# Performance work log

Hardware: AMD Instinct MI355X
Metric: run time of the kernel (lower is better)

Reference implementation:

```python
import jax, jax.numpy as jnp
import numpy as np

B, T, D_IN, N, O = 64, 512, 256, 1024, 128


def setup_inputs() -> dict:
    key = jax.random.key(0)
    k1, k2, k3, k4, k5 = jax.random.split(key, 5)
    X = jax.random.normal(k1, (B, T, D_IN), dtype=jnp.float32)
    # scale recurrent/input weights so tanh does not fully saturate
    Win = jax.random.normal(k2, (D_IN, N), dtype=jnp.float32) / np.sqrt(D_IN)
    W = jax.random.normal(k3, (N, N), dtype=jnp.float32) / np.sqrt(N)
    Wout = jax.random.normal(k4, (N, O), dtype=jnp.float32) / np.sqrt(N)
    bout = jax.random.normal(k5, (O,), dtype=jnp.float32)
    return {"X": X, "Win": Win, "W": W, "Wout": Wout, "bout": bout}


def reference(X, Win, W, Wout, bout):
    # Faithful to Model.evaluate:
    #   s[:, 0] = 0
    #   out = s @ Wout + bout
    b, t, _ = X.shape
    n = W.shape[0]
    s0 = jnp.zeros((b, n), dtype=X.dtype)

    def step(s, x):  # s: [B,N], x: [B,D_in]
        s_new = jnp.tanh(s @ W + x @ Win)
        return s_new, s_new

    xs = jnp.swapaxes(X[:, : t - 1, :], 0, 1)  # [T-1, B, D_in]
    _, s_seq = jax.lax.scan(step, s0, xs)  # [T-1, B, N]
    s = jnp.concatenate([s0[None], s_seq], axis=0)  # [T, B, N]
    s = jnp.swapaxes(s, 0, 1)  # [B, T, N]
    out = s @ Wout + bout  # [B, T, O]
    return (s, out)
```

## Files before the change

kernel.cpp:

```cpp
#include <hip/hip_runtime.h>

#define B_ 64
#define T_ 512
#define DIN_ 256
#define N_ 1024
#define O_ 128

using half8 = __attribute__((ext_vector_type(8))) _Float16;
using f32x4 = __attribute__((ext_vector_type(4))) float;
typedef unsigned long long ull;

__device__ __forceinline__ half8 cvt8(float4 a, float4 b) {
    half8 h;
    h[0] = (_Float16)a.x; h[1] = (_Float16)a.y; h[2] = (_Float16)a.z; h[3] = (_Float16)a.w;
    h[4] = (_Float16)b.x; h[5] = (_Float16)b.y; h[6] = (_Float16)b.z; h[7] = (_Float16)b.w;
    return h;
}

__device__ __forceinline__ float fast_tanh(float x) {
    float ax = __builtin_fabsf(x);
    float e  = __expf(-2.0f * ax);
    float r  = __fdividef(1.0f - e, 1.0f + e);
    return x < 0.0f ? -r : r;
}

__global__ void init_kernel(unsigned int* sent) {
    sent[threadIdx.x] = 0u;
}

__global__ __launch_bounds__(512, 1) void rnn_kernel(
    const float* __restrict__ X,
    const float* __restrict__ W,
    const float* __restrict__ Win,
    float* __restrict__ s_out,
    _Float16* __restrict__ exch,
    unsigned int* __restrict__ sent)
{
    const int bs   = blockIdx.x & 3;
    const int cg   = blockIdx.x >> 2;
    const int tid  = threadIdx.x;
    const int wave = tid >> 6;
    const int lane = tid & 63;
    const int l15  = lane & 15;
    const int quad = lane >> 4;
    const int col0 = cg * 128 + wave * 16;
    const int arow = bs * 16 + l15;
    const int crow = bs * 16 + quad * 4;

    __shared__ _Float16 slab[16 * 1032];

    half8 wf[32];
    for (int p = 0; p < 8; ++p) {
        const int c = tid & 15, k0 = tid >> 4;
        const int wc = cg * 128 + p * 16 + c;
        for (int k = k0; k < N_; k += 32)
            slab[c * 1032 + k] = (_Float16)W[(size_t)k * N_ + wc];
        __syncthreads();
        if (wave == p) {
            #pragma unroll
            for (int kb = 0; kb < 32; ++kb)
                wf[kb] = *(const half8*)&slab[l15 * 1032 + kb * 32 + quad * 8];
        }
        __syncthreads();
    }
    half8 winf[8];
    for (int p = 0; p < 8; ++p) {
        const int c = tid & 15, k0 = tid >> 4;
        const int wc = cg * 128 + p * 16 + c;
        for (int k = k0; k < DIN_; k += 32)
            slab[c * 1032 + k] = (_Float16)Win[(size_t)k * N_ + wc];
        __syncthreads();
        if (wave == p) {
            #pragma unroll
            for (int kb = 0; kb < 8; ++kb)
                winf[kb] = *(const half8*)&slab[l15 * 1032 + kb * 32 + quad * 8];
        }
        __syncthreads();
    }

    #pragma unroll
    for (int i = 0; i < 4; ++i) {
        int e = i * 512 + tid;
        int r = e >> 7, c = e & 127;
        s_out[(size_t)(bs * 16 + r) * T_ * N_ + cg * 128 + c] = 0.0f;
    }

    f32x4 u = {0.f, 0.f, 0.f, 0.f};
    {
        const float* xp = X + (size_t)arow * T_ * DIN_ + quad * 8;
        #pragma unroll
        for (int kb = 0; kb < 8; ++kb) {
            float4 x0 = *(const float4*)(xp + kb * 32);
            float4 x1 = *(const float4*)(xp + kb * 32 + 4);
            u = __builtin_amdgcn_mfma_f32_16x16x32_f16(cvt8(x0, x1), winf[kb], u, 0, 0, 0);
        }
    }

    const int col   = col0 + l15;
    const int ebase = (col >> 5) * 512 + ((col >> 3) & 3) * 128 + quad * 32 + (col & 7);

    unsigned int* sp = sent + bs * 64;
    const int mysent = cg * 8 + wave;

    for (int t = 1; t < T_; ++t) {
        f32x4 acc0 = u;
        f32x4 acc1 = {0.f, 0.f, 0.f, 0.f};
        f32x4 acc2 = {0.f, 0.f, 0.f, 0.f};
        f32x4 acc3 = {0.f, 0.f, 0.f, 0.f};

        if (t >= 2) {
            const unsigned want = (unsigned)(t - 1);
            for (;;) {
                unsigned v = __hip_atomic_load(&sp[lane], __ATOMIC_RELAXED,
                                               __HIP_MEMORY_SCOPE_AGENT);
                if (__all((int)(v >= want))) break;
            }

            const ull* ep = (const ull*)(exch + (size_t)(bs * 2 + ((t - 1) & 1)) * 16384);
            ull r0 = __hip_atomic_load(&ep[tid],        __ATOMIC_RELAXED, __HIP_MEMORY_SCOPE_AGENT);
            ull r1 = __hip_atomic_load(&ep[tid + 512],  __ATOMIC_RELAXED, __HIP_MEMORY_SCOPE_AGENT);
            ull r2 = __hip_atomic_load(&ep[tid + 1024], __ATOMIC_RELAXED, __HIP_MEMORY_SCOPE_AGENT);
            ull r3 = __hip_atomic_load(&ep[tid + 1536], __ATOMIC_RELAXED, __HIP_MEMORY_SCOPE_AGENT);
            ull r4 = __hip_atomic_load(&ep[tid + 2048], __ATOMIC_RELAXED, __HIP_MEMORY_SCOPE_AGENT);
            ull r5 = __hip_atomic_load(&ep[tid + 2560], __ATOMIC_RELAXED, __HIP_MEMORY_SCOPE_AGENT);
            ull r6 = __hip_atomic_load(&ep[tid + 3072], __ATOMIC_RELAXED, __HIP_MEMORY_SCOPE_AGENT);
            ull r7 = __hip_atomic_load(&ep[tid + 3584], __ATOMIC_RELAXED, __HIP_MEMORY_SCOPE_AGENT);

            asm volatile("s_barrier" ::: "memory");

            ull* lp = (ull*)slab;
            lp[tid]        = r0;
            lp[tid + 512]  = r1;
            lp[tid + 1024] = r2;
            lp[tid + 1536] = r3;
            lp[tid + 2048] = r4;
            lp[tid + 2560] = r5;
            lp[tid + 3072] = r6;
            lp[tid + 3584] = r7;
            asm volatile("s_waitcnt lgkmcnt(0)\n\ts_barrier" ::: "memory");

            #pragma unroll
            for (int kb = 0; kb < 32; ++kb) {
                half8 a = *(const half8*)&slab[kb * 512 + lane * 8];
                if ((kb & 3) == 0)      acc0 = __builtin_amdgcn_mfma_f32_16x16x32_f16(a, wf[kb], acc0, 0, 0, 0);
                else if ((kb & 3) == 1) acc1 = __builtin_amdgcn_mfma_f32_16x16x32_f16(a, wf[kb], acc1, 0, 0, 0);
                else if ((kb & 3) == 2) acc2 = __builtin_amdgcn_mfma_f32_16x16x32_f16(a, wf[kb], acc2, 0, 0, 0);
                else                    acc3 = __builtin_amdgcn_mfma_f32_16x16x32_f16(a, wf[kb], acc3, 0, 0, 0);
            }
        }

        float v4[4];
        #pragma unroll
        for (int r = 0; r < 4; ++r)
            v4[r] = fast_tanh(acc0[r] + acc1[r] + acc2[r] + acc3[r]);

        _Float16* eb = exch + (size_t)(bs * 2 + (t & 1)) * 16384;
        #pragma unroll
        for (int r = 0; r < 4; ++r) {
            union { _Float16 h; unsigned short s; } cv;
            cv.h = (_Float16)v4[r];
            __hip_atomic_store((unsigned short*)(eb + ebase + r * 8), cv.s,
                               __ATOMIC_RELAXED, __HIP_MEMORY_SCOPE_AGENT);
        }
        asm volatile("s_waitcnt vmcnt(0)" ::: "memory");
        if (lane == 0)
            __hip_atomic_store(&sp[mysent], (unsigned int)t,
                               __ATOMIC_RELAXED, __HIP_MEMORY_SCOPE_AGENT);

        #pragma unroll
        for (int r = 0; r < 4; ++r)
            s_out[(size_t)(crow + r) * T_ * N_ + (size_t)t * N_ + col] = v4[r];

        f32x4 un = {0.f, 0.f, 0.f, 0.f};
        if (t < T_ - 1) {
            const float* xp = X + ((size_t)arow * T_ + t) * DIN_ + quad * 8;
            #pragma unroll
            for (int kb = 0; kb < 8; ++kb) {
                float4 x0 = *(const float4*)(xp + kb * 32);
                float4 x1 = *(const float4*)(xp + kb * 32 + 4);
                un = __builtin_amdgcn_mfma_f32_16x16x32_f16(cvt8(x0, x1), winf[kb], un, 0, 0, 0);
            }
        }
        u = un;
    }
}

__global__ __launch_bounds__(256, 2) void out_gemm(
    const float* __restrict__ s_in,
    const float* __restrict__ Wout,
    const float* __restrict__ bout,
    float* __restrict__ outp)
{
    const int m0   = blockIdx.x * 128;
    const int tid  = threadIdx.x;
    const int wave = tid >> 6;
    const int lane = tid & 63;
    const int l15  = lane & 15;
    const int quad = lane >> 4;

    __shared__ _Float16 WoT[128][40];

    f32x4 acc[2][8];
    #pragma unroll
    for (int mf = 0; mf < 2; ++mf)
        #pragma unroll
        for (int nt = 0; nt < 8; ++nt) acc[mf][nt] = f32x4{0.f, 0.f, 0.f, 0.f};
    float bv[8];
    #pragma unroll
    for (int nt = 0; nt < 8; ++nt) bv[nt] = bout[nt * 16 + l15];

    for (int kb = 0; kb < 32; ++kb) {
        __syncthreads();
        #pragma unroll
        for (int i = 0; i < 16; ++i) {
            int e = i * 256 + tid;
            int c = e & 127, kk = e >> 7;
            WoT[c][kk] = (_Float16)Wout[(size_t)(kb * 32 + kk) * O_ + c];
        }
        __syncthreads();

        #pragma unroll
        for (int mf = 0; mf < 2; ++mf) {
            const float* ap = s_in + (size_t)(m0 + wave * 32 + mf * 16 + l15) * N_ + kb * 32 + quad * 8;
            float4 a0 = *(const float4*)ap;
            float4 a1 = *(const float4*)(ap + 4);
            half8 a = cvt8(a0, a1);
            #pragma unroll
            for (int nt = 0; nt < 8; ++nt) {
                half8 b = *(const half8*)&WoT[nt * 16 + l15][quad * 8];
                acc[mf][nt] = __builtin_amdgcn_mfma_f32_16x16x32_f16(a, b, acc[mf][nt], 0, 0, 0);
            }
        }
    }

    #pragma unroll
    for (int mf = 0; mf < 2; ++mf) {
        float* op = outp + (size_t)(m0 + wave * 32 + mf * 16 + quad * 4) * O_ + l15;
        #pragma unroll
        for (int nt = 0; nt < 8; ++nt)
            #pragma unroll
            for (int r = 0; r < 4; ++r)
                op[(size_t)r * O_ + nt * 16] = acc[mf][nt][r] + bv[nt];
    }
}

extern "C" void kernel_launch(void* const* d_in, const int* in_sizes, int n_in,
                              void* d_out, int out_size, void* d_ws, size_t ws_size,
                              hipStream_t stream) {
    const float* X    = (const float*)d_in[0];
    const float* Win  = (const float*)d_in[1];
    const float* W    = (const float*)d_in[2];
    const float* Wout = (const float*)d_in[3];
    const float* bout = (const float*)d_in[4];

    float* s_out = (float*)d_out;
    float* outp  = s_out + (size_t)B_ * T_ * N_;

    unsigned int* sent = (unsigned int*)d_ws;
    _Float16* exch = (_Float16*)((char*)d_ws + 4096);

    init_kernel<<<1, 256, 0, stream>>>(sent);
    rnn_kernel<<<32, 512, 0, stream>>>(X, W, Win, s_out, exch, sent);
    out_gemm<<<256, 256, 0, stream>>>(s_out, Wout, bout, outp);
}
```

Before: 3.219 ms.

## Load exchanged state directly into MFMA fragments, drop LDS staging and barriers

Each wave now reads its A-operand fragments for the recurrent matmul straight from the global exchange buffer with 64-bit atomic loads, double-buffered across groups of four k-blocks so loads overlap MFMAs. This removes the LDS staging copy and the two workgroup barriers per timestep. The publishing side stages each wave's 16x16 fp16 tile through a per-wave LDS region and writes it out as one coalesced 64-bit store per lane, replacing four scattered 16-bit stores. In exchange, every wave now reads the whole state vector from global/L2 itself (8x the traffic per block), and the layout change must match the reader's indexing.

```diff
diff --git a/kernel.cpp b/kernel.cpp
--- a/kernel.cpp
+++ b/kernel.cpp
@@ -22,6 +22,13 @@
     float e  = __expf(-2.0f * ax);
     float r  = __fdividef(1.0f - e, 1.0f + e);
     return x < 0.0f ? -r : r;
+}
+
+__device__ __forceinline__ half8 ldh8(const ull* ep, int kb, int li) {
+    union { ull q[2]; half8 h; } ua;
+    ua.q[0] = __hip_atomic_load(&ep[kb * 128 + li],     __ATOMIC_RELAXED, __HIP_MEMORY_SCOPE_AGENT);
+    ua.q[1] = __hip_atomic_load(&ep[kb * 128 + li + 1], __ATOMIC_RELAXED, __HIP_MEMORY_SCOPE_AGENT);
+    return ua.h;
 }
 
 __global__ void init_kernel(unsigned int* sent) {
@@ -47,7 +54,7 @@
     const int arow = bs * 16 + l15;
     const int crow = bs * 16 + quad * 4;
 
-    __shared__ _Float16 slab[16 * 1032];
+    __shared__ __align__(16) _Float16 slab[16 * 1032];
 
     half8 wf[32];
     for (int p = 0; p < 8; ++p) {
@@ -96,17 +103,18 @@
         }
     }
 
-    const int col   = col0 + l15;
-    const int ebase = (col >> 5) * 512 + ((col >> 3) & 3) * 128 + quad * 32 + (col & 7);
-
+    const int col = col0 + l15;
     unsigned int* sp = sent + bs * 64;
     const int mysent = cg * 8 + wave;
+    _Float16* pw = slab + wave * 256;
+    const int li = lane * 2;
 
     for (int t = 1; t < T_; ++t) {
-        f32x4 acc0 = u;
-        f32x4 acc1 = {0.f, 0.f, 0.f, 0.f};
-        f32x4 acc2 = {0.f, 0.f, 0.f, 0.f};
-        f32x4 acc3 = {0.f, 0.f, 0.f, 0.f};
+        f32x4 acc[4];
+        acc[0] = u;
+        acc[1] = f32x4{0.f, 0.f, 0.f, 0.f};
+        acc[2] = f32x4{0.f, 0.f, 0.f, 0.f};
+        acc[3] = f32x4{0.f, 0.f, 0.f, 0.f};
 
         if (t >= 2) {
             const unsigned want = (unsigned)(t - 1);
@@ -117,51 +125,37 @@
             }
 
             const ull* ep = (const ull*)(exch + (size_t)(bs * 2 + ((t - 1) & 1)) * 16384);
-            ull r0 = __hip_atomic_load(&ep[tid],        __ATOMIC_RELAXED, __HIP_MEMORY_SCOPE_AGENT);
-            ull r1 = __hip_atomic_load(&ep[tid + 512],  __ATOMIC_RELAXED, __HIP_MEMORY_SCOPE_AGENT);
-            ull r2 = __hip_atomic_load(&ep[tid + 1024], __ATOMIC_RELAXED, __HIP_MEMORY_SCOPE_AGENT);
-            ull r3 = __hip_atomic_load(&ep[tid + 1536], __ATOMIC_RELAXED, __HIP_MEMORY_SCOPE_AGENT);
-            ull r4 = __hip_atomic_load(&ep[tid + 2048], __ATOMIC_RELAXED, __HIP_MEMORY_SCOPE_AGENT);
-            ull r5 = __hip_atomic_load(&ep[tid + 2560], __ATOMIC_RELAXED, __HIP_MEMORY_SCOPE_AGENT);
-            ull r6 = __hip_atomic_load(&ep[tid + 3072], __ATOMIC_RELAXED, __HIP_MEMORY_SCOPE_AGENT);
-            ull r7 = __hip_atomic_load(&ep[tid + 3584], __ATOMIC_RELAXED, __HIP_MEMORY_SCOPE_AGENT);
-
-            asm volatile("s_barrier" ::: "memory");
-
-            ull* lp = (ull*)slab;
-            lp[tid]        = r0;
-            lp[tid + 512]  = r1;
-            lp[tid + 1024] = r2;
-            lp[tid + 1536] = r3;
-            lp[tid + 2048] = r4;
-            lp[tid + 2560] = r5;
-            lp[tid + 3072] = r6;
-            lp[tid + 3584] = r7;
-            asm volatile("s_waitcnt lgkmcnt(0)\n\ts_barrier" ::: "memory");
-
-            #pragma unroll
-            for (int kb = 0; kb < 32; ++kb) {
-                half8 a = *(const half8*)&slab[kb * 512 + lane * 8];
-                if ((kb & 3) == 0)      acc0 = __builtin_amdgcn_mfma_f32_16x16x32_f16(a, wf[kb], acc0, 0, 0, 0);
-                else if ((kb & 3) == 1) acc1 = __builtin_amdgcn_mfma_f32_16x16x32_f16(a, wf[kb], acc1, 0, 0, 0);
-                else if ((kb & 3) == 2) acc2 = __builtin_amdgcn_mfma_f32_16x16x32_f16(a, wf[kb], acc2, 0, 0, 0);
-                else                    acc3 = __builtin_amdgcn_mfma_f32_16x16x32_f16(a, wf[kb], acc3, 0, 0, 0);
+            half8 ab[2][4];
+            #pragma unroll
+            for (int j = 0; j < 4; ++j) ab[0][j] = ldh8(ep, j, li);
+            #pragma unroll
+            for (int g = 0; g < 8; ++g) {
+                if (g < 7) {
+                    #pragma unroll
+                    for (int j = 0; j < 4; ++j)
+                        ab[(g + 1) & 1][j] = ldh8(ep, (g + 1) * 4 + j, li);
+                }
+                #pragma unroll
+                for (int j = 0; j < 4; ++j)
+                    acc[j] = __builtin_amdgcn_mfma_f32_16x16x32_f16(
+                        ab[g & 1][j], wf[g * 4 + j], acc[j], 0, 0, 0);
             }
         }
 
         float v4[4];
         #pragma unroll
         for (int r = 0; r < 4; ++r)
-            v4[r] = fast_tanh(acc0[r] + acc1[r] + acc2[r] + acc3[r]);
-
-        _Float16* eb = exch + (size_t)(bs * 2 + (t & 1)) * 16384;
-        #pragma unroll
-        for (int r = 0; r < 4; ++r) {
-            union { _Float16 h; unsigned short s; } cv;
-            cv.h = (_Float16)v4[r];
-            __hip_atomic_store((unsigned short*)(eb + ebase + r * 8), cv.s,
-                               __ATOMIC_RELAXED, __HIP_MEMORY_SCOPE_AGENT);
-        }
+            v4[r] = fast_tanh(acc[0][r] + acc[1][r] + acc[2][r] + acc[3][r]);
+
+        asm volatile("s_waitcnt lgkmcnt(0)" ::: "memory");
+        #pragma unroll
+        for (int r = 0; r < 4; ++r)
+            pw[(l15 >> 3) * 128 + (quad * 4 + r) * 8 + (l15 & 7)] = (_Float16)v4[r];
+        asm volatile("s_waitcnt lgkmcnt(0)" ::: "memory");
+        ull chunk = *(const ull*)(pw + lane * 4);
+        char* eb = (char*)exch + (size_t)(bs * 2 + (t & 1)) * 32768;
+        __hip_atomic_store((ull*)(eb + (size_t)col0 * 32 + (size_t)lane * 8), chunk,
+                           __ATOMIC_RELAXED, __HIP_MEMORY_SCOPE_AGENT);
         asm volatile("s_waitcnt vmcnt(0)" ::: "memory");
         if (lane == 0)
             __hip_atomic_store(&sp[mysent], (unsigned int)t,
```

Result: slower. 4.798 ms (+49.0%).

## Overlap input projection with exchange, coalesce publish via LDS, single-wave polling

Applied to the files above, without the earlier changes.

Changes the recurrent step's cross-block synchronisation and publishing. Only wave 0 polls the global sentinels and then releases the other waves through an LDS flag, replacing the s_barrier. The exchange slab is double-buffered. Each wave stages its fp16 outputs in LDS and publishes them with one coalesced 64-bit store per lane instead of four scattered 16-bit atomic stores. The X@Win product for the next step is computed from register-prefetched X while the exchange loads are in flight, which costs extra registers and relies on LDS spin-flag ordering being correct.

```diff
diff --git a/kernel.cpp b/kernel.cpp
--- a/kernel.cpp
+++ b/kernel.cpp
@@ -47,19 +47,23 @@
     const int arow = bs * 16 + l15;
     const int crow = bs * 16 + quad * 4;
 
-    __shared__ _Float16 slab[16 * 1032];
+    __shared__ __align__(16) _Float16 smem[2 * 16 * 1024 + 8 * 256 + 8];
+    _Float16* slab0 = smem;
+    _Float16* slab1 = smem + 16384;
+    _Float16* pub   = smem + 32768;
+    volatile int* fl = (volatile int*)(smem + 32768 + 2048);
 
     half8 wf[32];
     for (int p = 0; p < 8; ++p) {
         const int c = tid & 15, k0 = tid >> 4;
         const int wc = cg * 128 + p * 16 + c;
         for (int k = k0; k < N_; k += 32)
-            slab[c * 1032 + k] = (_Float16)W[(size_t)k * N_ + wc];
+            smem[c * 1032 + k] = (_Float16)W[(size_t)k * N_ + wc];
         __syncthreads();
         if (wave == p) {
             #pragma unroll
             for (int kb = 0; kb < 32; ++kb)
-                wf[kb] = *(const half8*)&slab[l15 * 1032 + kb * 32 + quad * 8];
+                wf[kb] = *(const half8*)&smem[l15 * 1032 + kb * 32 + quad * 8];
         }
         __syncthreads();
     }
@@ -68,15 +72,16 @@
         const int c = tid & 15, k0 = tid >> 4;
         const int wc = cg * 128 + p * 16 + c;
         for (int k = k0; k < DIN_; k += 32)
-            slab[c * 1032 + k] = (_Float16)Win[(size_t)k * N_ + wc];
+            smem[c * 1032 + k] = (_Float16)Win[(size_t)k * N_ + wc];
         __syncthreads();
         if (wave == p) {
             #pragma unroll
             for (int kb = 0; kb < 8; ++kb)
-                winf[kb] = *(const half8*)&slab[l15 * 1032 + kb * 32 + quad * 8];
-        }
-        __syncthreads();
-    }
+                winf[kb] = *(const half8*)&smem[l15 * 1032 + kb * 32 + quad * 8];
+        }
+        __syncthreads();
+    }
+    if (tid == 0) *fl = 0;
 
     #pragma unroll
     for (int i = 0; i < 4; ++i) {
@@ -84,8 +89,10 @@
         int r = e >> 7, c = e & 127;
         s_out[(size_t)(bs * 16 + r) * T_ * N_ + cg * 128 + c] = 0.0f;
     }
+    __syncthreads();
 
     f32x4 u = {0.f, 0.f, 0.f, 0.f};
+    float4 xr[16];
     {
         const float* xp = X + (size_t)arow * T_ * DIN_ + quad * 8;
         #pragma unroll
@@ -94,26 +101,41 @@
             float4 x1 = *(const float4*)(xp + kb * 32 + 4);
             u = __builtin_amdgcn_mfma_f32_16x16x32_f16(cvt8(x0, x1), winf[kb], u, 0, 0, 0);
         }
-    }
-
-    const int col   = col0 + l15;
-    const int ebase = (col >> 5) * 512 + ((col >> 3) & 3) * 128 + quad * 32 + (col & 7);
-
+        const float* xq = xp + DIN_;
+        #pragma unroll
+        for (int kb = 0; kb < 8; ++kb) {
+            xr[2 * kb]     = *(const float4*)(xq + kb * 32);
+            xr[2 * kb + 1] = *(const float4*)(xq + kb * 32 + 4);
+        }
+    }
+
+    const int col = col0 + l15;
     unsigned int* sp = sent + bs * 64;
     const int mysent = cg * 8 + wave;
+    _Float16* pw = pub + wave * 256;
 
     for (int t = 1; t < T_; ++t) {
         f32x4 acc0 = u;
         f32x4 acc1 = {0.f, 0.f, 0.f, 0.f};
         f32x4 acc2 = {0.f, 0.f, 0.f, 0.f};
         f32x4 acc3 = {0.f, 0.f, 0.f, 0.f};
+        f32x4 un   = {0.f, 0.f, 0.f, 0.f};
+        _Float16* slab = ((t - 1) & 1) ? slab1 : slab0;
 
         if (t >= 2) {
-            const unsigned want = (unsigned)(t - 1);
-            for (;;) {
-                unsigned v = __hip_atomic_load(&sp[lane], __ATOMIC_RELAXED,
-                                               __HIP_MEMORY_SCOPE_AGENT);
-                if (__all((int)(v >= want))) break;
+            const int want = t - 1;
+            if (wave == 0) {
+                unsigned va = __hip_atomic_load(&sp[lane], __ATOMIC_RELAXED,
+                                                __HIP_MEMORY_SCOPE_AGENT);
+                for (;;) {
+                    unsigned vb = __hip_atomic_load(&sp[lane], __ATOMIC_RELAXED,
+                                                    __HIP_MEMORY_SCOPE_AGENT);
+                    if (__all((int)(va >= (unsigned)want))) break;
+                    va = vb;
+                }
+                if (lane == 0) *fl = want;
+            } else {
+                while (*fl < want) { }
             }
 
             const ull* ep = (const ull*)(exch + (size_t)(bs * 2 + ((t - 1) & 1)) * 16384);
@@ -126,7 +148,12 @@
             ull r6 = __hip_atomic_load(&ep[tid + 3072], __ATOMIC_RELAXED, __HIP_MEMORY_SCOPE_AGENT);
             ull r7 = __hip_atomic_load(&ep[tid + 3584], __ATOMIC_RELAXED, __HIP_MEMORY_SCOPE_AGENT);
 
-            asm volatile("s_barrier" ::: "memory");
+            if (t < T_ - 1) {
+                #pragma unroll
+                for (int kb = 0; kb < 8; ++kb)
+                    un = __builtin_amdgcn_mfma_f32_16x16x32_f16(
+                        cvt8(xr[2 * kb], xr[2 * kb + 1]), winf[kb], un, 0, 0, 0);
+            }
 
             ull* lp = (ull*)slab;
             lp[tid]        = r0;
@@ -147,6 +174,11 @@
                 else if ((kb & 3) == 2) acc2 = __builtin_amdgcn_mfma_f32_16x16x32_f16(a, wf[kb], acc2, 0, 0, 0);
                 else                    acc3 = __builtin_amdgcn_mfma_f32_16x16x32_f16(a, wf[kb], acc3, 0, 0, 0);
             }
+        } else {
+            #pragma unroll
+            for (int kb = 0; kb < 8; ++kb)
+                un = __builtin_amdgcn_mfma_f32_16x16x32_f16(
+                    cvt8(xr[2 * kb], xr[2 * kb + 1]), winf[kb], un, 0, 0, 0);
         }
 
         float v4[4];
@@ -154,14 +186,15 @@
         for (int r = 0; r < 4; ++r)
             v4[r] = fast_tanh(acc0[r] + acc1[r] + acc2[r] + acc3[r]);
 
-        _Float16* eb = exch + (size_t)(bs * 2 + (t & 1)) * 16384;
-        #pragma unroll
-        for (int r = 0; r < 4; ++r) {
-            union { _Float16 h; unsigned short s; } cv;
-            cv.h = (_Float16)v4[r];
-            __hip_atomic_store((unsigned short*)(eb + ebase + r * 8), cv.s,
-                               __ATOMIC_RELAXED, __HIP_MEMORY_SCOPE_AGENT);
-        }
+        asm volatile("s_waitcnt lgkmcnt(0)" ::: "memory");
+        #pragma unroll
+        for (int r = 0; r < 4; ++r)
+            pw[(l15 >> 3) * 128 + (quad * 4 + r) * 8 + (l15 & 7)] = (_Float16)v4[r];
+        asm volatile("s_waitcnt lgkmcnt(0)" ::: "memory");
+        ull chunk = *(const ull*)(pw + lane * 4);
+        char* eb = (char*)exch + (size_t)(bs * 2 + (t & 1)) * 32768;
+        __hip_atomic_store((ull*)(eb + (size_t)col0 * 32 + (size_t)lane * 8), chunk,
+                           __ATOMIC_RELAXED, __HIP_MEMORY_SCOPE_AGENT);
         asm volatile("s_waitcnt vmcnt(0)" ::: "memory");
         if (lane == 0)
             __hip_atomic_store(&sp[mysent], (unsigned int)t,
@@ -171,14 +204,12 @@
         for (int r = 0; r < 4; ++r)
             s_out[(size_t)(crow + r) * T_ * N_ + (size_t)t * N_ + col] = v4[r];
 
-        f32x4 un = {0.f, 0.f, 0.f, 0.f};
-        if (t < T_ - 1) {
-            const float* xp = X + ((size_t)arow * T_ + t) * DIN_ + quad * 8;
+        if (t < T_ - 2) {
+            const float* xq = X + ((size_t)arow * T_ + t + 1) * DIN_ + quad * 8;
             #pragma unroll
             for (int kb = 0; kb < 8; ++kb) {
-                float4 x0 = *(const float4*)(xp + kb * 32);
-                float4 x1 = *(const float4*)(xp + kb * 32 + 4);
-                un = __builtin_amdgcn_mfma_f32_16x16x32_f16(cvt8(x0, x1), winf[kb], un, 0, 0, 0);
+                xr[2 * kb]     = *(const float4*)(xq + kb * 32);
+                xr[2 * kb + 1] = *(const float4*)(xq + kb * 32 + 4);
             }
         }
         u = un;
```

New measurement: 4.004 ms. 24.4% more time.
